# Kernel tuning notes

Measured on AMD Instinct MI355X. Metric: run time of the kernel, lower is better.

The kernel has to match this reference:

```python
import jax, jax.numpy as jnp
import numpy as np

T, B, I, H = 8192, 1, 1024, 1024


def _lstm_layer(x, W_ih, W_hh, b_ih, b_hh):
    # x: [T, B, I]; torch gate order: input, forget, cell(g), output
    Hh = W_hh.shape[1]
    xg = jnp.einsum('tbi,gi->tbg', x, W_ih) + b_ih + b_hh  # [T, B, 4H]

    def step(carry, xg_t):
        h, c = carry
        gates = xg_t + h @ W_hh.T  # [B, 4H]
        i, f, g, o = jnp.split(gates, 4, axis=-1)
        c = jax.nn.sigmoid(f) * c + jax.nn.sigmoid(i) * jnp.tanh(g)
        h = jax.nn.sigmoid(o) * jnp.tanh(c)
        return (h, c), h

    h0 = jnp.zeros((x.shape[1], Hh), x.dtype)
    (_, _), ys = jax.lax.scan(step, (h0, h0), xg)
    return ys  # [T, B, H]


def setup_inputs() -> dict:
    key = jax.random.key(0)
    ks = jax.random.split(key, 9)
    s = 0.02
    return {
        'inputs': jax.random.normal(ks[0], (T, B, I), dtype=jnp.float32),
        'W_ih0': jax.random.normal(ks[1], (4 * H, I), dtype=jnp.float32) * s,
        'W_hh0': jax.random.normal(ks[2], (4 * H, H), dtype=jnp.float32) * s,
        'b_ih0': jax.random.normal(ks[3], (4 * H,), dtype=jnp.float32) * s,
        'b_hh0': jax.random.normal(ks[4], (4 * H,), dtype=jnp.float32) * s,
        'W_ih1': jax.random.normal(ks[5], (4 * H, H), dtype=jnp.float32) * s,
        'W_hh1': jax.random.normal(ks[6], (4 * H, H), dtype=jnp.float32) * s,
        'b_ih1': jax.random.normal(ks[7], (4 * H,), dtype=jnp.float32) * s,
        'b_hh1': jax.random.normal(ks[8], (4 * H,), dtype=jnp.float32) * s,
    }


def reference(inputs, W_ih0, W_hh0, b_ih0, b_hh0, W_ih1, W_hh1, b_ih1, b_hh1):
    # 2-layer LSTM, zero initial state, dropout omitted (eval semantics)
    y0 = _lstm_layer(inputs, W_ih0, W_hh0, b_ih0, b_hh0)
    y1 = _lstm_layer(y0, W_ih1, W_hh1, b_ih1, b_hh1)
    return y1[-1]  # [B, H] — last timestep of top layer
```

## Files before the change

### kernel.cpp

```cpp
#include <hip/hip_runtime.h>

#define T_STEPS 8192
#define HID 1024
#define G4 4096
#define NBLK 128
#define NTHR 512
#define NSLOT 8

typedef unsigned int uint32;

struct Comm {
    uint32 hA[NSLOT][HID];
    uint32 hB[NSLOT][HID];
};

#define LD_AG  __HIP_MEMORY_SCOPE_AGENT

__device__ inline float sigm(float x) { return 1.0f / (1.0f + __expf(-x)); }
__device__ inline float tanh_f(float x) {
    x = fminf(fmaxf(x, -15.f), 15.f);
    float e = __expf(-2.0f * x);
    return (1.0f - e) / (1.0f + e);
}
__device__ inline uint32 tagf(float f, uint32 tg) {
    union { float f; uint32 u; } a; a.f = f;
    return (a.u & ~15u) | tg;
}

__global__ __launch_bounds__(256)
void gemm_xg(const float* __restrict__ A, const float* __restrict__ W,
             const float* __restrict__ bi, const float* __restrict__ bh,
             float* __restrict__ out)
{
    __shared__ float As[16][65];
    __shared__ float Bs[16][65];
    const int tid = threadIdx.x;
    const int m0 = blockIdx.y * 64, n0 = blockIdx.x * 64;
    const int tm = tid & 15, tn = tid >> 4;
    const int row = tid >> 2, q = tid & 3;
    float acc[4][4] = {{0.f}};
    for (int k0 = 0; k0 < HID; k0 += 16) {
        float4 a = *(const float4*)(A + (size_t)(m0 + row) * HID + k0 + q * 4);
        float4 b = *(const float4*)(W + (size_t)(n0 + row) * HID + k0 + q * 4);
        __syncthreads();
        As[q*4+0][row] = a.x; As[q*4+1][row] = a.y; As[q*4+2][row] = a.z; As[q*4+3][row] = a.w;
        Bs[q*4+0][row] = b.x; Bs[q*4+1][row] = b.y; Bs[q*4+2][row] = b.z; Bs[q*4+3][row] = b.w;
        __syncthreads();
#pragma unroll
        for (int kk = 0; kk < 16; ++kk) {
            float av[4], bv[4];
#pragma unroll
            for (int i = 0; i < 4; ++i) { av[i] = As[kk][tm*4+i]; bv[i] = Bs[kk][tn*4+i]; }
#pragma unroll
            for (int i = 0; i < 4; ++i)
#pragma unroll
                for (int j = 0; j < 4; ++j) acc[i][j] += av[i] * bv[j];
        }
    }
#pragma unroll
    for (int i = 0; i < 4; ++i) {
        int m = m0 + tm * 4 + i;
#pragma unroll
        for (int j = 0; j < 4; ++j) {
            int n = n0 + tn * 4 + j;
            float v = acc[i][j] + bi[n] + bh[n];
            int jd = n & (HID - 1), gate = n >> 10;
            out[(size_t)m * G4 + (jd >> 3) * 32 + (jd & 7) * 4 + gate] = v;
        }
    }
}

__device__ inline void poll8(const uint32* __restrict__ buf, uint32 tg,
                             int lane, float* __restrict__ lds)
{
    uint32 v[8];
    for (;;) {
#pragma unroll
        for (int r = 0; r < 8; ++r)
            v[r] = __hip_atomic_load(&buf[r * 64 + lane], __ATOMIC_RELAXED, LD_AG);
        bool ok = true;
#pragma unroll
        for (int r = 0; r < 8; ++r) ok &= ((v[r] & 15u) == tg);
        if (__all(ok)) break;
    }
#pragma unroll
    for (int r = 0; r < 8; ++r) {
        union { uint32 u; float f; } c; c.u = v[r];
        lds[r * 64 + lane] = c.f;
    }
}

__device__ inline void scan16(const uint32* __restrict__ buf, uint32 tg, int lane)
{
    uint32 v[16];
    for (;;) {
        bool ok = true;
#pragma unroll
        for (int r = 0; r < 16; ++r)
            v[r] = __hip_atomic_load(&buf[r * 64 + lane], __ATOMIC_RELAXED, LD_AG);
#pragma unroll
        for (int r = 0; r < 16; ++r) ok &= ((v[r] & 15u) == tg);
        if (__all(ok)) break;
    }
}

__global__ __launch_bounds__(NTHR)
void lstm_fused(const float* __restrict__ Whh0, const float* __restrict__ xg,
                const float* __restrict__ Wih1, const float* __restrict__ Whh1,
                const float* __restrict__ bih1, const float* __restrict__ bhh1,
                float* __restrict__ outF, Comm* __restrict__ cm)
{
    __shared__ float Wl[32 * HID];
    __shared__ float hlA[HID];
    __shared__ float hlB[HID];
    const int blk = blockIdx.x, tid = threadIdx.x;
    const int wave = tid >> 6, lane = tid & 63;
    const int kb = (blk < NBLK) ? blk : blk - NBLK;

    {
        const float* Wsrc = (blk < NBLK) ? Whh0 : Whh1;
#pragma unroll
        for (int i = 0; i < 16; ++i) {
            int l = i * NTHR + tid;
            int r = l >> 8, c = l & 255;
            int w = r >> 2, g = r & 3;
            ((float4*)(Wl + r * HID))[c] =
                ((const float4*)(Wsrc + (size_t)(g * HID + 8 * kb + w) * HID))[c];
        }
    }
    for (int i = tid; i < HID; i += NTHR) { hlA[i] = 0.f; hlB[i] = 0.f; }

    if (blk < NBLK) {
        const int k = kb;
        float c_state = 0.f;
        float nx0 = 0.f, nx1 = 0.f, nx2 = 0.f, nx3 = 0.f;
        if (lane == 0) {
            const float* xp = xg + k * 32 + wave * 4;
            nx0 = xp[0]; nx1 = xp[1]; nx2 = xp[2]; nx3 = xp[3];
        }
        __syncthreads();

        for (int t = 0; t < T_STEPS; ++t) {
            float x0 = nx0, x1 = nx1, x2 = nx2, x3 = nx3;
            if (lane == 0 && t + 1 < T_STEPS) {
                const float* xp = xg + (size_t)(t + 1) * G4 + k * 32 + wave * 4;
                nx0 = xp[0]; nx1 = xp[1]; nx2 = xp[2]; nx3 = xp[3];
            }
            float a0 = 0.f, a1 = 0.f, a2 = 0.f, a3 = 0.f;
            const float* wb = Wl + wave * 4 * HID;
#pragma unroll 4
            for (int u = 0; u < 16; ++u) {
                float hv = hlA[u * 64 + lane];
                a0 += wb[0 * HID + u * 64 + lane] * hv;
                a1 += wb[1 * HID + u * 64 + lane] * hv;
                a2 += wb[2 * HID + u * 64 + lane] * hv;
                a3 += wb[3 * HID + u * 64 + lane] * hv;
            }
#pragma unroll
            for (int off = 32; off > 0; off >>= 1) {
                a0 += __shfl_xor(a0, off, 64);
                a1 += __shfl_xor(a1, off, 64);
                a2 += __shfl_xor(a2, off, 64);
                a3 += __shfl_xor(a3, off, 64);
            }
            if (lane == 0) {
                float ig = sigm(x0 + a0);
                float fg = sigm(x1 + a1);
                float gg = tanh_f(x2 + a2);
                float og = sigm(x3 + a3);
                c_state = fg * c_state + ig * gg;
                float h = og * tanh_f(c_state);
                __hip_atomic_store(&cm->hA[t & 7][8 * k + wave],
                                   tagf(h, (t >> 3) & 15), __ATOMIC_RELAXED, LD_AG);
            }
            if (t == T_STEPS - 1) break;
            __syncthreads();
            if (wave == 0) {
                poll8(cm->hA[t & 7], (t >> 3) & 15, lane, hlA);
            } else if (wave == 1) {
                poll8(cm->hA[t & 7] + 512, (t >> 3) & 15, lane, hlA + 512);
            } else if (wave == 2 && t >= 4) {
                scan16(cm->hB[(t - 4) & 7], ((t - 4) >> 3) & 15, lane);
            }
            __syncthreads();
        }
    } else {
        const int j = 8 * kb + wave;
        float wreg[4][16];
#pragma unroll
        for (int g = 0; g < 4; ++g)
#pragma unroll
            for (int u = 0; u < 16; ++u)
                wreg[g][u] = Wih1[(size_t)(g * HID + j) * HID + u * 64 + lane];
        float bia[4];
#pragma unroll
        for (int g = 0; g < 4; ++g)
            bia[g] = bih1[g * HID + j] + bhh1[g * HID + j];
        float c_state = 0.f;
        __syncthreads();

        for (int t = 0; t < T_STEPS; ++t) {
            if (wave == 0) {
                poll8(cm->hA[t & 7], (t >> 3) & 15, lane, hlA);
            } else if (wave == 1) {
                poll8(cm->hA[t & 7] + 512, (t >> 3) & 15, lane, hlA + 512);
            } else if (wave == 2 && t >= 1) {
                poll8(cm->hB[(t - 1) & 7], ((t - 1) >> 3) & 15, lane, hlB);
            } else if (wave == 3 && t >= 1) {
                poll8(cm->hB[(t - 1) & 7] + 512, ((t - 1) >> 3) & 15, lane, hlB + 512);
            }
            __syncthreads();
            float a0 = 0.f, a1 = 0.f, a2 = 0.f, a3 = 0.f;
            const float* wb = Wl + wave * 4 * HID;
#pragma unroll
            for (int u = 0; u < 16; ++u) {
                float h0v = hlA[u * 64 + lane];
                float h1v = hlB[u * 64 + lane];
                a0 += wb[0 * HID + u * 64 + lane] * h1v + wreg[0][u] * h0v;
                a1 += wb[1 * HID + u * 64 + lane] * h1v + wreg[1][u] * h0v;
                a2 += wb[2 * HID + u * 64 + lane] * h1v + wreg[2][u] * h0v;
                a3 += wb[3 * HID + u * 64 + lane] * h1v + wreg[3][u] * h0v;
            }
#pragma unroll
            for (int off = 32; off > 0; off >>= 1) {
                a0 += __shfl_xor(a0, off, 64);
                a1 += __shfl_xor(a1, off, 64);
                a2 += __shfl_xor(a2, off, 64);
                a3 += __shfl_xor(a3, off, 64);
            }
            if (lane == 0) {
                float ig = sigm(bia[0] + a0);
                float fg = sigm(bia[1] + a1);
                float gg = tanh_f(bia[2] + a2);
                float og = sigm(bia[3] + a3);
                c_state = fg * c_state + ig * gg;
                float h = og * tanh_f(c_state);
                if (t == T_STEPS - 1)
                    outF[j] = h;
                else
                    __hip_atomic_store(&cm->hB[t & 7][j],
                                       tagf(h, (t >> 3) & 15), __ATOMIC_RELAXED, LD_AG);
            }
            if (t == T_STEPS - 1) break;
            __syncthreads();
        }
    }
}

extern "C" void kernel_launch(void* const* d_in, const int* in_sizes, int n_in,
                              void* d_out, int out_size, void* d_ws, size_t ws_size,
                              hipStream_t stream)
{
    const float* x    = (const float*)d_in[0];
    const float* Wih0 = (const float*)d_in[1];
    const float* Whh0 = (const float*)d_in[2];
    const float* bih0 = (const float*)d_in[3];
    const float* bhh0 = (const float*)d_in[4];
    const float* Wih1 = (const float*)d_in[5];
    const float* Whh1 = (const float*)d_in[6];
    const float* bih1 = (const float*)d_in[7];
    const float* bhh1 = (const float*)d_in[8];

    char* ws = (char*)d_ws;
    float* xg = (float*)ws;
    Comm*  cm = (Comm*)(ws + 134217728);

    (void)hipMemsetAsync(ws + 134217728, 0xFF, sizeof(Comm), stream);

    dim3 gg(G4 / 64, T_STEPS / 64);
    gemm_xg<<<gg, 256, 0, stream>>>(x, Wih0, bih0, bhh0, xg);
    lstm_fused<<<2 * NBLK, NTHR, 0, stream>>>(Whh0, xg, Wih1, Whh1, bih1, bhh1,
                                              (float*)d_out, cm);
}
```

Before: 36.23 ms.

## Specialize waves into compute and poller roles with double-buffered LDS flags

```diff
diff --git a/kernel.cpp b/kernel.cpp
--- a/kernel.cpp
+++ b/kernel.cpp
@@ -8,13 +8,15 @@
 #define NSLOT 8
 
 typedef unsigned int uint32;
+typedef unsigned long long ull;
 
 struct Comm {
-    uint32 hA[NSLOT][HID];
-    uint32 hB[NSLOT][HID];
+    ull hA[NSLOT][HID / 2];
+    ull hB[NSLOT][HID / 2];
 };
 
 #define LD_AG  __HIP_MEMORY_SCOPE_AGENT
+#define LD_WG  __HIP_MEMORY_SCOPE_WORKGROUP
 
 __device__ inline float sigm(float x) { return 1.0f / (1.0f + __expf(-x)); }
 __device__ inline float tanh_f(float x) {
@@ -70,10 +72,9 @@
     }
 }
 
-__device__ inline void poll8(const uint32* __restrict__ buf, uint32 tg,
-                             int lane, float* __restrict__ lds)
+__device__ inline void detect8(const uint32* __restrict__ buf, uint32 tg,
+                               int lane, uint32 v[8])
 {
-    uint32 v[8];
     for (;;) {
 #pragma unroll
         for (int r = 0; r < 8; ++r)
@@ -81,25 +82,6 @@
         bool ok = true;
 #pragma unroll
         for (int r = 0; r < 8; ++r) ok &= ((v[r] & 15u) == tg);
-        if (__all(ok)) break;
-    }
-#pragma unroll
-    for (int r = 0; r < 8; ++r) {
-        union { uint32 u; float f; } c; c.u = v[r];
-        lds[r * 64 + lane] = c.f;
-    }
-}
-
-__device__ inline void scan16(const uint32* __restrict__ buf, uint32 tg, int lane)
-{
-    uint32 v[16];
-    for (;;) {
-        bool ok = true;
-#pragma unroll
-        for (int r = 0; r < 16; ++r)
-            v[r] = __hip_atomic_load(&buf[r * 64 + lane], __ATOMIC_RELAXED, LD_AG);
-#pragma unroll
-        for (int r = 0; r < 16; ++r) ok &= ((v[r] & 15u) == tg);
         if (__all(ok)) break;
     }
 }
@@ -111,14 +93,18 @@
                 float* __restrict__ outF, Comm* __restrict__ cm)
 {
     __shared__ float Wl[32 * HID];
-    __shared__ float hlA[HID];
-    __shared__ float hlB[HID];
+    __shared__ float hlA[2][HID];
+    __shared__ float hlB[2][HID];
+    __shared__ int flagAlo[2], flagAhi[2], flagBlo[2], flagBhi[2];
+    __shared__ int prog[4];
+    __shared__ int bpA;
     const int blk = blockIdx.x, tid = threadIdx.x;
     const int wave = tid >> 6, lane = tid & 63;
     const int kb = (blk < NBLK) ? blk : blk - NBLK;
+    const bool isL0 = (blk < NBLK);
 
     {
-        const float* Wsrc = (blk < NBLK) ? Whh0 : Whh1;
+        const float* Wsrc = isL0 ? Whh0 : Whh1;
 #pragma unroll
         for (int i = 0; i < 16; ++i) {
             int l = i * NTHR + tid;
@@ -128,121 +114,199 @@
                 ((const float4*)(Wsrc + (size_t)(g * HID + 8 * kb + w) * HID))[c];
         }
     }
-    for (int i = tid; i < HID; i += NTHR) { hlA[i] = 0.f; hlB[i] = 0.f; }
-
-    if (blk < NBLK) {
+    for (int i = tid; i < HID; i += NTHR) {
+        hlA[0][i] = 0.f; hlA[1][i] = 0.f; hlB[0][i] = 0.f; hlB[1][i] = 0.f;
+    }
+    if (tid == 0) {
+        flagAlo[0] = -2; flagAhi[0] = -2; flagAlo[1] = -1; flagAhi[1] = -1;
+        flagBlo[0] = -2; flagBhi[0] = -2; flagBlo[1] = -1; flagBhi[1] = -1;
+        prog[0] = prog[1] = prog[2] = prog[3] = -1;
+        bpA = -1;
+    }
+    __syncthreads();
+
+    if (isL0) {
         const int k = kb;
-        float c_state = 0.f;
-        float nx0 = 0.f, nx1 = 0.f, nx2 = 0.f, nx3 = 0.f;
-        if (lane == 0) {
-            const float* xp = xg + k * 32 + wave * 4;
-            nx0 = xp[0]; nx1 = xp[1]; nx2 = xp[2]; nx3 = xp[3];
-        }
-        __syncthreads();
-
-        for (int t = 0; t < T_STEPS; ++t) {
-            float x0 = nx0, x1 = nx1, x2 = nx2, x3 = nx3;
-            if (lane == 0 && t + 1 < T_STEPS) {
-                const float* xp = xg + (size_t)(t + 1) * G4 + k * 32 + wave * 4;
-                nx0 = xp[0]; nx1 = xp[1]; nx2 = xp[2]; nx3 = xp[3];
-            }
-            float a0 = 0.f, a1 = 0.f, a2 = 0.f, a3 = 0.f;
-            const float* wb = Wl + wave * 4 * HID;
+        if (wave < 4) {
+            float c0 = 0.f, c1 = 0.f;
+            float nx[8];
+            if (lane == 0) {
+                const float4* xp = (const float4*)(xg + k * 32 + 8 * wave);
+                float4 A = xp[0], B = xp[1];
+                nx[0]=A.x; nx[1]=A.y; nx[2]=A.z; nx[3]=A.w;
+                nx[4]=B.x; nx[5]=B.y; nx[6]=B.z; nx[7]=B.w;
+            }
+            const float* wb = Wl + (size_t)(8 * wave) * HID;
+            for (int t = 0; t < T_STEPS; ++t) {
+                const int pm = (t - 1) & 1;
+                while (__hip_atomic_load(&flagAlo[pm], __ATOMIC_ACQUIRE, LD_WG) < t - 1) {}
+                while (__hip_atomic_load(&flagAhi[pm], __ATOMIC_ACQUIRE, LD_WG) < t - 1) {}
+                float x[8];
+#pragma unroll
+                for (int i = 0; i < 8; ++i) x[i] = nx[i];
+                if (lane == 0 && t + 1 < T_STEPS) {
+                    const float4* xp = (const float4*)(xg + (size_t)(t + 1) * G4 + k * 32 + 8 * wave);
+                    float4 A = xp[0], B = xp[1];
+                    nx[0]=A.x; nx[1]=A.y; nx[2]=A.z; nx[3]=A.w;
+                    nx[4]=B.x; nx[5]=B.y; nx[6]=B.z; nx[7]=B.w;
+                }
+                float a[8] = {0.f,0.f,0.f,0.f,0.f,0.f,0.f,0.f};
 #pragma unroll 4
-            for (int u = 0; u < 16; ++u) {
-                float hv = hlA[u * 64 + lane];
-                a0 += wb[0 * HID + u * 64 + lane] * hv;
-                a1 += wb[1 * HID + u * 64 + lane] * hv;
-                a2 += wb[2 * HID + u * 64 + lane] * hv;
-                a3 += wb[3 * HID + u * 64 + lane] * hv;
-            }
-#pragma unroll
-            for (int off = 32; off > 0; off >>= 1) {
-                a0 += __shfl_xor(a0, off, 64);
-                a1 += __shfl_xor(a1, off, 64);
-                a2 += __shfl_xor(a2, off, 64);
-                a3 += __shfl_xor(a3, off, 64);
-            }
-            if (lane == 0) {
-                float ig = sigm(x0 + a0);
-                float fg = sigm(x1 + a1);
-                float gg = tanh_f(x2 + a2);
-                float og = sigm(x3 + a3);
-                c_state = fg * c_state + ig * gg;
-                float h = og * tanh_f(c_state);
-                __hip_atomic_store(&cm->hA[t & 7][8 * k + wave],
-                                   tagf(h, (t >> 3) & 15), __ATOMIC_RELAXED, LD_AG);
-            }
-            if (t == T_STEPS - 1) break;
-            __syncthreads();
-            if (wave == 0) {
-                poll8(cm->hA[t & 7], (t >> 3) & 15, lane, hlA);
-            } else if (wave == 1) {
-                poll8(cm->hA[t & 7] + 512, (t >> 3) & 15, lane, hlA + 512);
-            } else if (wave == 2 && t >= 4) {
-                scan16(cm->hB[(t - 4) & 7], ((t - 4) >> 3) & 15, lane);
-            }
-            __syncthreads();
+                for (int u = 0; u < 16; ++u) {
+                    float hv = hlA[pm][u * 64 + lane];
+#pragma unroll
+                    for (int r = 0; r < 8; ++r)
+                        a[r] += wb[r * HID + u * 64 + lane] * hv;
+                }
+#pragma unroll
+                for (int off = 32; off > 0; off >>= 1)
+#pragma unroll
+                    for (int r = 0; r < 8; ++r) a[r] += __shfl_xor(a[r], off, 64);
+                while (__hip_atomic_load(&bpA, __ATOMIC_RELAXED, LD_WG) < t - 8) {}
+                if (lane == 0) {
+                    const uint32 tg = (t >> 3) & 15;
+                    float i0 = sigm(x[0] + a[0]), f0 = sigm(x[1] + a[1]);
+                    float g0 = tanh_f(x[2] + a[2]), o0 = sigm(x[3] + a[3]);
+                    c0 = f0 * c0 + i0 * g0;
+                    float h0 = o0 * tanh_f(c0);
+                    float i1 = sigm(x[4] + a[4]), f1 = sigm(x[5] + a[5]);
+                    float g1 = tanh_f(x[6] + a[6]), o1 = sigm(x[7] + a[7]);
+                    c1 = f1 * c1 + i1 * g1;
+                    float h1 = o1 * tanh_f(c1);
+                    ull pk = (ull)tagf(h0, tg) | ((ull)tagf(h1, tg) << 32);
+                    __hip_atomic_store(&cm->hA[t & 7][4 * k + wave], pk,
+                                       __ATOMIC_RELAXED, LD_AG);
+                }
+            }
+        } else if (wave == 4 || wave == 5) {
+            const int half = wave - 4;
+            int* flg = half ? flagAhi : flagAlo;
+            for (int t = 0; t <= T_STEPS - 2; ++t) {
+                uint32 v[8];
+                detect8((const uint32*)cm->hA[t & 7] + half * 512, (t >> 3) & 15, lane, v);
+                float* dst = hlA[t & 1] + half * 512;
+#pragma unroll
+                for (int r = 0; r < 8; ++r) {
+                    union { uint32 u; float f; } c; c.u = v[r];
+                    dst[r * 64 + lane] = c.f;
+                }
+                if (lane == 0)
+                    __hip_atomic_store(&flg[t & 1], t, __ATOMIC_RELEASE, LD_WG);
+            }
+        } else if (wave == 6) {
+            for (int s = 0; s <= T_STEPS - 9; ++s) {
+                const uint32 tg = (s >> 3) & 15;
+                const uint32* hb = (const uint32*)cm->hB[s & 7];
+                for (;;) {
+                    uint32 v[16]; bool ok = true;
+#pragma unroll
+                    for (int r = 0; r < 16; ++r)
+                        v[r] = __hip_atomic_load(&hb[r * 64 + lane], __ATOMIC_RELAXED, LD_AG);
+#pragma unroll
+                    for (int r = 0; r < 16; ++r)
+                        ok &= (((v[r] & 15u) - tg) & 15u) < 8u;
+                    if (__all(ok)) break;
+                }
+                if (lane == 0)
+                    __hip_atomic_store(&bpA, s, __ATOMIC_RELEASE, LD_WG);
+            }
         }
     } else {
-        const int j = 8 * kb + wave;
-        float wreg[4][16];
-#pragma unroll
-        for (int g = 0; g < 4; ++g)
-#pragma unroll
-            for (int u = 0; u < 16; ++u)
-                wreg[g][u] = Wih1[(size_t)(g * HID + j) * HID + u * 64 + lane];
-        float bia[4];
-#pragma unroll
-        for (int g = 0; g < 4; ++g)
-            bia[g] = bih1[g * HID + j] + bhh1[g * HID + j];
-        float c_state = 0.f;
-        __syncthreads();
-
-        for (int t = 0; t < T_STEPS; ++t) {
-            if (wave == 0) {
-                poll8(cm->hA[t & 7], (t >> 3) & 15, lane, hlA);
-            } else if (wave == 1) {
-                poll8(cm->hA[t & 7] + 512, (t >> 3) & 15, lane, hlA + 512);
-            } else if (wave == 2 && t >= 1) {
-                poll8(cm->hB[(t - 1) & 7], ((t - 1) >> 3) & 15, lane, hlB);
-            } else if (wave == 3 && t >= 1) {
-                poll8(cm->hB[(t - 1) & 7] + 512, ((t - 1) >> 3) & 15, lane, hlB + 512);
-            }
-            __syncthreads();
-            float a0 = 0.f, a1 = 0.f, a2 = 0.f, a3 = 0.f;
-            const float* wb = Wl + wave * 4 * HID;
-#pragma unroll
-            for (int u = 0; u < 16; ++u) {
-                float h0v = hlA[u * 64 + lane];
-                float h1v = hlB[u * 64 + lane];
-                a0 += wb[0 * HID + u * 64 + lane] * h1v + wreg[0][u] * h0v;
-                a1 += wb[1 * HID + u * 64 + lane] * h1v + wreg[1][u] * h0v;
-                a2 += wb[2 * HID + u * 64 + lane] * h1v + wreg[2][u] * h0v;
-                a3 += wb[3 * HID + u * 64 + lane] * h1v + wreg[3][u] * h0v;
-            }
-#pragma unroll
-            for (int off = 32; off > 0; off >>= 1) {
-                a0 += __shfl_xor(a0, off, 64);
-                a1 += __shfl_xor(a1, off, 64);
-                a2 += __shfl_xor(a2, off, 64);
-                a3 += __shfl_xor(a3, off, 64);
-            }
-            if (lane == 0) {
-                float ig = sigm(bia[0] + a0);
-                float fg = sigm(bia[1] + a1);
-                float gg = tanh_f(bia[2] + a2);
-                float og = sigm(bia[3] + a3);
-                c_state = fg * c_state + ig * gg;
-                float h = og * tanh_f(c_state);
-                if (t == T_STEPS - 1)
-                    outF[j] = h;
-                else
-                    __hip_atomic_store(&cm->hB[t & 7][j],
-                                       tagf(h, (t >> 3) & 15), __ATOMIC_RELAXED, LD_AG);
-            }
-            if (t == T_STEPS - 1) break;
-            __syncthreads();
+        if (wave < 4) {
+            const int j0 = 8 * kb + 2 * wave;
+            float wreg[128];
+#pragma unroll
+            for (int c2 = 0; c2 < 2; ++c2)
+#pragma unroll
+                for (int g = 0; g < 4; ++g)
+#pragma unroll
+                    for (int u = 0; u < 16; ++u)
+                        wreg[(c2 * 4 + g) * 16 + u] =
+                            Wih1[(size_t)(g * HID + j0 + c2) * HID + u * 64 + lane];
+            float bia[8];
+#pragma unroll
+            for (int c2 = 0; c2 < 2; ++c2)
+#pragma unroll
+                for (int g = 0; g < 4; ++g)
+                    bia[c2 * 4 + g] = bih1[g * HID + j0 + c2] + bhh1[g * HID + j0 + c2];
+            float c0 = 0.f, c1 = 0.f;
+            const float* wb = Wl + (size_t)(8 * wave) * HID;
+            for (int t = 0; t < T_STEPS; ++t) {
+                const int pa = t & 1, pb = (t - 1) & 1;
+                while (__hip_atomic_load(&flagAlo[pa], __ATOMIC_ACQUIRE, LD_WG) < t) {}
+                while (__hip_atomic_load(&flagAhi[pa], __ATOMIC_ACQUIRE, LD_WG) < t) {}
+                while (__hip_atomic_load(&flagBlo[pb], __ATOMIC_ACQUIRE, LD_WG) < t - 1) {}
+                while (__hip_atomic_load(&flagBhi[pb], __ATOMIC_ACQUIRE, LD_WG) < t - 1) {}
+                float a[8] = {0.f,0.f,0.f,0.f,0.f,0.f,0.f,0.f};
+#pragma unroll 4
+                for (int u = 0; u < 16; ++u) {
+                    float h0v = hlA[pa][u * 64 + lane];
+                    float h1v = hlB[pb][u * 64 + lane];
+#pragma unroll
+                    for (int r = 0; r < 8; ++r)
+                        a[r] += wb[r * HID + u * 64 + lane] * h1v + wreg[r * 16 + u] * h0v;
+                }
+                if (lane == 0)
+                    __hip_atomic_store(&prog[wave], t, __ATOMIC_RELEASE, LD_WG);
+#pragma unroll
+                for (int off = 32; off > 0; off >>= 1)
+#pragma unroll
+                    for (int r = 0; r < 8; ++r) a[r] += __shfl_xor(a[r], off, 64);
+                if (lane == 0) {
+                    const uint32 tg = (t >> 3) & 15;
+                    float i0 = sigm(bia[0] + a[0]), f0 = sigm(bia[1] + a[1]);
+                    float g0 = tanh_f(bia[2] + a[2]), o0 = sigm(bia[3] + a[3]);
+                    c0 = f0 * c0 + i0 * g0;
+                    float h0 = o0 * tanh_f(c0);
+                    float i1 = sigm(bia[4] + a[4]), f1 = sigm(bia[5] + a[5]);
+                    float g1 = tanh_f(bia[6] + a[6]), o1 = sigm(bia[7] + a[7]);
+                    c1 = f1 * c1 + i1 * g1;
+                    float h1 = o1 * tanh_f(c1);
+                    if (t == T_STEPS - 1) {
+                        float2 o; o.x = h0; o.y = h1;
+                        *(float2*)(outF + j0) = o;
+                    } else {
+                        ull pk = (ull)tagf(h0, tg) | ((ull)tagf(h1, tg) << 32);
+                        __hip_atomic_store(&cm->hB[t & 7][4 * kb + wave], pk,
+                                           __ATOMIC_RELAXED, LD_AG);
+                    }
+                }
+            }
+        } else if (wave == 4 || wave == 5) {
+            const int half = wave - 4;
+            int* flg = half ? flagAhi : flagAlo;
+            for (int t = 0; t <= T_STEPS - 1; ++t) {
+                uint32 v[8];
+                detect8((const uint32*)cm->hA[t & 7] + half * 512, (t >> 3) & 15, lane, v);
+                for (;;) {
+                    bool ok = (lane >= 4) ||
+                        (__hip_atomic_load(&prog[lane], __ATOMIC_ACQUIRE, LD_WG) >= t - 2);
+                    if (__all(ok)) break;
+                }
+                float* dst = hlA[t & 1] + half * 512;
+#pragma unroll
+                for (int r = 0; r < 8; ++r) {
+                    union { uint32 u; float f; } c; c.u = v[r];
+                    dst[r * 64 + lane] = c.f;
+                }
+                if (lane == 0)
+                    __hip_atomic_store(&flg[t & 1], t, __ATOMIC_RELEASE, LD_WG);
+            }
+        } else {
+            const int half = wave - 6;
+            int* flg = half ? flagBhi : flagBlo;
+            for (int s = 0; s <= T_STEPS - 2; ++s) {
+                uint32 v[8];
+                detect8((const uint32*)cm->hB[s & 7] + half * 512, (s >> 3) & 15, lane, v);
+                float* dst = hlB[s & 1] + half * 512;
+#pragma unroll
+                for (int r = 0; r < 8; ++r) {
+                    union { uint32 u; float f; } c; c.u = v[r];
+                    dst[r * 64 + lane] = c.f;
+                }
+                if (lane == 0)
+                    __hip_atomic_store(&flg[s & 1], s, __ATOMIC_RELEASE, LD_WG);
+            }
         }
     }
 }
```

Result: slower. 72.82 ms (+101.0%).

## Double-buffer LDS hidden state and decouple layer-1 backpressure polling

Applied to the files above, without the earlier changes.

```diff
diff --git a/kernel.cpp b/kernel.cpp
--- a/kernel.cpp
+++ b/kernel.cpp
@@ -5,7 +5,7 @@
 #define G4 4096
 #define NBLK 128
 #define NTHR 512
-#define NSLOT 8
+#define NSLOT 16
 
 typedef unsigned int uint32;
 
@@ -15,6 +15,7 @@
 };
 
 #define LD_AG  __HIP_MEMORY_SCOPE_AGENT
+#define LD_WG  __HIP_MEMORY_SCOPE_WORKGROUP
 
 __device__ inline float sigm(float x) { return 1.0f / (1.0f + __expf(-x)); }
 __device__ inline float tanh_f(float x) {
@@ -70,38 +71,29 @@
     }
 }
 
-__device__ inline void poll8(const uint32* __restrict__ buf, uint32 tg,
-                             int lane, float* __restrict__ lds)
-{
-    uint32 v[8];
-    for (;;) {
-#pragma unroll
-        for (int r = 0; r < 8; ++r)
-            v[r] = __hip_atomic_load(&buf[r * 64 + lane], __ATOMIC_RELAXED, LD_AG);
-        bool ok = true;
-#pragma unroll
-        for (int r = 0; r < 8; ++r) ok &= ((v[r] & 15u) == tg);
-        if (__all(ok)) break;
-    }
-#pragma unroll
-    for (int r = 0; r < 8; ++r) {
-        union { uint32 u; float f; } c; c.u = v[r];
-        lds[r * 64 + lane] = c.f;
-    }
-}
-
-__device__ inline void scan16(const uint32* __restrict__ buf, uint32 tg, int lane)
-{
-    uint32 v[16];
+__device__ inline void detect4(const uint32* __restrict__ buf, uint32 tg,
+                               int lane, uint32 v[4])
+{
     for (;;) {
         bool ok = true;
 #pragma unroll
-        for (int r = 0; r < 16; ++r)
+        for (int r = 0; r < 4; ++r)
             v[r] = __hip_atomic_load(&buf[r * 64 + lane], __ATOMIC_RELAXED, LD_AG);
 #pragma unroll
-        for (int r = 0; r < 16; ++r) ok &= ((v[r] & 15u) == tg);
+        for (int r = 0; r < 4; ++r) ok &= ((v[r] & 15u) == tg);
         if (__all(ok)) break;
     }
+}
+
+__device__ inline bool try_scan16(const uint32* __restrict__ buf, uint32 tg, int lane)
+{
+    uint32 v[16]; bool ok = true;
+#pragma unroll
+    for (int r = 0; r < 16; ++r)
+        v[r] = __hip_atomic_load(&buf[r * 64 + lane], __ATOMIC_RELAXED, LD_AG);
+#pragma unroll
+    for (int r = 0; r < 16; ++r) ok &= (((v[r] & 15u) - tg) & 15u) < 8u;
+    return __all(ok);
 }
 
 __global__ __launch_bounds__(NTHR)
@@ -111,14 +103,16 @@
                 float* __restrict__ outF, Comm* __restrict__ cm)
 {
     __shared__ float Wl[32 * HID];
-    __shared__ float hlA[HID];
-    __shared__ float hlB[HID];
+    __shared__ float hlA[2][HID];
+    __shared__ float hlB[2][HID];
+    __shared__ int bpA;
     const int blk = blockIdx.x, tid = threadIdx.x;
     const int wave = tid >> 6, lane = tid & 63;
     const int kb = (blk < NBLK) ? blk : blk - NBLK;
+    const bool isL0 = (blk < NBLK);
 
     {
-        const float* Wsrc = (blk < NBLK) ? Whh0 : Whh1;
+        const float* Wsrc = isL0 ? Whh0 : Whh1;
 #pragma unroll
         for (int i = 0; i < 16; ++i) {
             int l = i * NTHR + tid;
@@ -128,9 +122,13 @@
                 ((const float4*)(Wsrc + (size_t)(g * HID + 8 * kb + w) * HID))[c];
         }
     }
-    for (int i = tid; i < HID; i += NTHR) { hlA[i] = 0.f; hlB[i] = 0.f; }
-
-    if (blk < NBLK) {
+    for (int i = tid; i < HID; i += NTHR) {
+        hlA[0][i] = 0.f; hlA[1][i] = 0.f; hlB[0][i] = 0.f; hlB[1][i] = 0.f;
+    }
+    if (tid == 0) bpA = -1;
+    __syncthreads();
+
+    if (isL0) {
         const int k = kb;
         float c_state = 0.f;
         float nx0 = 0.f, nx1 = 0.f, nx2 = 0.f, nx3 = 0.f;
@@ -138,9 +136,10 @@
             const float* xp = xg + k * 32 + wave * 4;
             nx0 = xp[0]; nx1 = xp[1]; nx2 = xp[2]; nx3 = xp[3];
         }
-        __syncthreads();
+        int bp_next = 0;
 
         for (int t = 0; t < T_STEPS; ++t) {
+            const int pm = (t - 1) & 1;
             float x0 = nx0, x1 = nx1, x2 = nx2, x3 = nx3;
             if (lane == 0 && t + 1 < T_STEPS) {
                 const float* xp = xg + (size_t)(t + 1) * G4 + k * 32 + wave * 4;
@@ -150,7 +149,7 @@
             const float* wb = Wl + wave * 4 * HID;
 #pragma unroll 4
             for (int u = 0; u < 16; ++u) {
-                float hv = hlA[u * 64 + lane];
+                float hv = hlA[pm][u * 64 + lane];
                 a0 += wb[0 * HID + u * 64 + lane] * hv;
                 a1 += wb[1 * HID + u * 64 + lane] * hv;
                 a2 += wb[2 * HID + u * 64 + lane] * hv;
@@ -162,6 +161,12 @@
                 a1 += __shfl_xor(a1, off, 64);
                 a2 += __shfl_xor(a2, off, 64);
                 a3 += __shfl_xor(a3, off, 64);
+            }
+            if (t >= 16 &&
+                __hip_atomic_load(&bpA, __ATOMIC_RELAXED, LD_WG) < t - 16) {
+                const int s = t - 16;
+                while (!try_scan16((const uint32*)cm->hB[s & 15],
+                                   (s >> 4) & 15, lane)) {}
             }
             if (lane == 0) {
                 float ig = sigm(x0 + a0);
@@ -170,17 +175,28 @@
                 float og = sigm(x3 + a3);
                 c_state = fg * c_state + ig * gg;
                 float h = og * tanh_f(c_state);
-                __hip_atomic_store(&cm->hA[t & 7][8 * k + wave],
-                                   tagf(h, (t >> 3) & 15), __ATOMIC_RELAXED, LD_AG);
+                __hip_atomic_store(&cm->hA[t & 15][8 * k + wave],
+                                   tagf(h, (t >> 4) & 15), __ATOMIC_RELAXED, LD_AG);
             }
             if (t == T_STEPS - 1) break;
-            __syncthreads();
-            if (wave == 0) {
-                poll8(cm->hA[t & 7], (t >> 3) & 15, lane, hlA);
-            } else if (wave == 1) {
-                poll8(cm->hA[t & 7] + 512, (t >> 3) & 15, lane, hlA + 512);
-            } else if (wave == 2 && t >= 4) {
-                scan16(cm->hB[(t - 4) & 7], ((t - 4) >> 3) & 15, lane);
+            if (wave < 4) {
+                uint32 v[4];
+                detect4((const uint32*)cm->hA[t & 15] + wave * 256,
+                        (t >> 4) & 15, lane, v);
+                float* dst = hlA[t & 1] + wave * 256;
+#pragma unroll
+                for (int r = 0; r < 4; ++r) {
+                    union { uint32 u; float f; } c; c.u = v[r];
+                    dst[r * 64 + lane] = c.f;
+                }
+            } else if (wave == 4) {
+                for (int it = 0; it < 8 && bp_next <= t; ++it) {
+                    if (!try_scan16((const uint32*)cm->hB[bp_next & 15],
+                                    (bp_next >> 4) & 15, lane)) break;
+                    if (lane == 0)
+                        __hip_atomic_store(&bpA, bp_next, __ATOMIC_RELAXED, LD_WG);
+                    ++bp_next;
+                }
             }
             __syncthreads();
         }
@@ -197,25 +213,38 @@
         for (int g = 0; g < 4; ++g)
             bia[g] = bih1[g * HID + j] + bhh1[g * HID + j];
         float c_state = 0.f;
-        __syncthreads();
 
         for (int t = 0; t < T_STEPS; ++t) {
-            if (wave == 0) {
-                poll8(cm->hA[t & 7], (t >> 3) & 15, lane, hlA);
-            } else if (wave == 1) {
-                poll8(cm->hA[t & 7] + 512, (t >> 3) & 15, lane, hlA + 512);
-            } else if (wave == 2 && t >= 1) {
-                poll8(cm->hB[(t - 1) & 7], ((t - 1) >> 3) & 15, lane, hlB);
-            } else if (wave == 3 && t >= 1) {
-                poll8(cm->hB[(t - 1) & 7] + 512, ((t - 1) >> 3) & 15, lane, hlB + 512);
+            if (wave < 4) {
+                uint32 v[4];
+                detect4((const uint32*)cm->hA[t & 15] + wave * 256,
+                        (t >> 4) & 15, lane, v);
+                float* dst = hlA[t & 1] + wave * 256;
+#pragma unroll
+                for (int r = 0; r < 4; ++r) {
+                    union { uint32 u; float f; } c; c.u = v[r];
+                    dst[r * 64 + lane] = c.f;
+                }
+            } else if (t >= 1) {
+                const int q = wave - 4;
+                uint32 v[4];
+                detect4((const uint32*)cm->hB[(t - 1) & 15] + q * 256,
+                        ((t - 1) >> 4) & 15, lane, v);
+                float* dst = hlB[(t - 1) & 1] + q * 256;
+#pragma unroll
+                for (int r = 0; r < 4; ++r) {
+                    union { uint32 u; float f; } c; c.u = v[r];
+                    dst[r * 64 + lane] = c.f;
+                }
             }
             __syncthreads();
+            const int pa = t & 1, pb = (t - 1) & 1;
             float a0 = 0.f, a1 = 0.f, a2 = 0.f, a3 = 0.f;
             const float* wb = Wl + wave * 4 * HID;
-#pragma unroll
+#pragma unroll 4
             for (int u = 0; u < 16; ++u) {
-                float h0v = hlA[u * 64 + lane];
-                float h1v = hlB[u * 64 + lane];
+                float h0v = hlA[pa][u * 64 + lane];
+                float h1v = hlB[pb][u * 64 + lane];
                 a0 += wb[0 * HID + u * 64 + lane] * h1v + wreg[0][u] * h0v;
                 a1 += wb[1 * HID + u * 64 + lane] * h1v + wreg[1][u] * h0v;
                 a2 += wb[2 * HID + u * 64 + lane] * h1v + wreg[2][u] * h0v;
@@ -238,11 +267,9 @@
                 if (t == T_STEPS - 1)
                     outF[j] = h;
                 else
-                    __hip_atomic_store(&cm->hB[t & 7][j],
-                                       tagf(h, (t >> 3) & 15), __ATOMIC_RELAXED, LD_AG);
-            }
-            if (t == T_STEPS - 1) break;
-            __syncthreads();
+                    __hip_atomic_store(&cm->hB[t & 15][j],
+                                       tagf(h, (t >> 4) & 15), __ATOMIC_RELAXED, LD_AG);
+            }
         }
     }
 }
```

After: 107.9 ms. 198% more time.
